# Kernel optimization log

Measured on AMD Instinct MI355X. Metric: run time of the kernel, lower is better.

The kernel has to match this reference:

```python
import jax, jax.numpy as jnp
import numpy as np

H = 400   # hidden_size
V = 77    # vocab / window size
K = 10    # attention mixture components
OUT = 121
B, T, U = 64, 600, 50


def setup_inputs() -> dict:
    key = jax.random.key(0)
    ks = jax.random.split(key, 16)
    def p(k, shape, s=0.08):
        return jax.random.normal(k, shape, dtype=jnp.float32) * s
    # bias for kappa-increment chunk kept negative so kappa advances ~exp(-3)=0.05/step
    b_win = jnp.concatenate([jnp.zeros(2 * K, jnp.float32), jnp.full((K,), -3.0, jnp.float32)])
    return {
        "inputs": jax.random.normal(ks[0], (B, T, 3), dtype=jnp.float32),
        "text": jax.random.randint(ks[1], (B, U), 0, V),
        "text_mask": jnp.ones((B, U), jnp.float32),
        "h0": jnp.zeros((3, B, H), jnp.float32),
        "c0": jnp.zeros((3, B, H), jnp.float32),
        "prev_window_vec": jnp.zeros((B, 1, V), jnp.float32),
        "prev_kappa": jnp.zeros((B, K, 1), jnp.float32),
        "w_ih1": p(ks[2], (4 * H, 3 + V)), "w_hh1": p(ks[3], (4 * H, H)),
        "b_ih1": jnp.zeros((4 * H,), jnp.float32), "b_hh1": jnp.zeros((4 * H,), jnp.float32),
        "w_ih2": p(ks[4], (4 * H, 3 + V + H)), "w_hh2": p(ks[5], (4 * H, H)),
        "b_ih2": jnp.zeros((4 * H,), jnp.float32), "b_hh2": jnp.zeros((4 * H,), jnp.float32),
        "w_ih3": p(ks[6], (4 * H, 3 + V + H)), "w_hh3": p(ks[7], (4 * H, H)),
        "b_ih3": jnp.zeros((4 * H,), jnp.float32), "b_hh3": jnp.zeros((4 * H,), jnp.float32),
        "w_win": p(ks[8], (3 * K, H), 0.01), "b_win": b_win,
        "w_out": p(ks[9], (OUT, 3 * H)), "b_out": jnp.zeros((OUT,), jnp.float32),
    }


def lstm_cell(x, h, c, Wih, Whh, bih, bhh):
    # PyTorch gate order: i, f, g, o
    g = x @ Wih.T + bih + h @ Whh.T + bhh
    i, f, gg, o = jnp.split(g, 4, axis=-1)
    c = jax.nn.sigmoid(f) * c + jax.nn.sigmoid(i) * jnp.tanh(gg)
    h = jax.nn.sigmoid(o) * jnp.tanh(c)
    return h, c


def reference(inputs, text, text_mask, h0, c0, prev_window_vec, prev_kappa,
              w_ih1, w_hh1, b_ih1, b_hh1, w_ih2, w_hh2, b_ih2, b_hh2,
              w_ih3, w_hh3, b_ih3, b_hh3, w_win, b_win, w_out, b_out):
    enc = jax.nn.one_hot(text, V, dtype=jnp.float32)            # [B,U,V]
    u = jnp.arange(U, dtype=jnp.float32)                         # [U]

    def step1(carry, x_t):
        h, c, wv, kappa = carry                                  # h,c:[B,H] wv:[B,V] kappa:[B,K]
        xi = jnp.concatenate([x_t, wv], axis=-1)                 # [B,3+V]
        h, c = lstm_cell(xi, h, c, w_ih1, w_hh1, b_ih1, b_hh1)
        mix = jnp.exp(h @ w_win.T + b_win)                       # [B,3K]
        alpha, beta, dk = jnp.split(mix, 3, axis=-1)             # each [B,K]
        kappa = kappa + dk
        phi = jnp.sum(alpha[:, :, None] * jnp.exp(-beta[:, :, None] * (kappa[:, :, None] - u) ** 2), axis=1)  # [B,U]
        phi = phi * text_mask
        wv = jnp.einsum('bu,buv->bv', phi, enc)                  # [B,V]
        return (h, c, wv, kappa), (h, wv)

    carry0 = (h0[0], c0[0], prev_window_vec[:, 0, :], prev_kappa[:, :, 0])
    (h1, c1, _, kappa_last), (hid1, wvec) = jax.lax.scan(step1, carry0, jnp.swapaxes(inputs, 0, 1))
    hid1 = jnp.swapaxes(hid1, 0, 1)                              # [B,T,H]
    wvec = jnp.swapaxes(wvec, 0, 1)                              # [B,T,V]

    def run_lstm(x, h, c, Wih, Whh, bih, bhh):
        def step(carry, x_t):
            h, c = carry
            h, c = lstm_cell(x_t, h, c, Wih, Whh, bih, bhh)
            return (h, c), h
        _, hs = jax.lax.scan(step, (h, c), jnp.swapaxes(x, 0, 1))
        return jnp.swapaxes(hs, 0, 1)

    hid2 = run_lstm(jnp.concatenate([inputs, hid1, wvec], axis=-1), h0[1], c0[1], w_ih2, w_hh2, b_ih2, b_hh2)
    hid3 = run_lstm(jnp.concatenate([inputs, hid2, wvec], axis=-1), h0[2], c0[2], w_ih3, w_hh3, b_ih3, b_hh3)
    y_hat = jnp.concatenate([hid1, hid2, hid3], axis=-1) @ w_out.T + b_out  # [B,T,121]
    return y_hat, wvec, kappa_last[:, :, None]
```

## Files before the change

kernel.cpp:

```cpp
#include <hip/hip_runtime.h>
#include <cstdint>
#include <cstddef>
#include <cstring>

using u32 = unsigned int;
typedef _Float16 h2 __attribute__((ext_vector_type(2)));
typedef _Float16 h4 __attribute__((ext_vector_type(4)));
typedef _Float16 h8 __attribute__((ext_vector_type(8)));
typedef float f32x4 __attribute__((ext_vector_type(4)));

constexpr int B_=64, T_=600, U_=50, V_=77, H_=400, OUT_=121;
constexpr int G1=50, GPA=16, G2=50, G3=50, GOUT=8;
constexpr int NBLK = G1+GPA+G2+G3+GOUT;
constexpr u32 CNT0=50, CNT1=16, CNT2=50, CNT3=50;

constexpr size_t FLAGS_B = 0;
constexpr size_t FLAGS_SZ = 4ull*600*64;
constexpr size_t W1WG   = 15ull*32*4*8;
constexpr size_t W1F_B  = FLAGS_SZ;
constexpr size_t W2WG   = 28ull*32*4*8;
constexpr size_t W2F_B  = W1F_B + 50ull*W1WG*2;
constexpr size_t W3F_B  = W2F_B + 50ull*W2WG*2;
constexpr size_t WOWG   = 300ull*32*16;
constexpr size_t WOF_B  = W3F_B + 50ull*W2WG*2;
constexpr size_t WWFWG  = 200ull*32;
constexpr size_t WWF_B  = WOF_B + 8ull*WOWG*2;
constexpr size_t WWMWG  = 15ull*32*4*8;
constexpr size_t WWM_B  = WWF_B + 16ull*WWFWG*4;
constexpr size_t FWV_B  = WWM_B + 50ull*WWMWG*2;
constexpr size_t FH1_B  = FWV_B + 600ull*64*40*4;
constexpr size_t FH2_B  = FH1_B + 600ull*64*200*4;
constexpr size_t FH3_B  = FH2_B + 600ull*64*200*4;

constexpr int SW1 = 184;
constexpr int SW2 = 232;
constexpr int SWO = 244;
constexpr int SMEM_BYTES = 59392;

struct P {
  const float *x, *tmask, *h0, *c0, *pwv, *pkap;
  const int *text;
  const float *wih1,*whh1,*bih1,*bhh1;
  const float *wih2,*whh2,*bih2,*bhh2;
  const float *wih3,*whh3,*bih3,*bhh3;
  const float *wwin,*bwin,*wout,*bout;
  float *out_y,*out_wv,*out_kap;
  _Float16 *w1f,*w2f,*w3f,*wof,*wwm;
  u32 *wwf;
  u32 *fwv,*fh1,*fh2,*fh3;
  u32 *flags;
};

__device__ __forceinline__ u32 ldc_u(const u32* p) {
  return __hip_atomic_load((u32*)p, __ATOMIC_RELAXED, __HIP_MEMORY_SCOPE_AGENT);
}
__device__ __forceinline__ void stc_u(u32* p, u32 v) {
  __hip_atomic_store(p, v, __ATOMIC_RELAXED, __HIP_MEMORY_SCOPE_AGENT);
}
__device__ __forceinline__ float sigm(float x) { return 1.f/(1.f+__expf(-x)); }
__device__ __forceinline__ h2 pk16(float a, float b) {
  auto t = __builtin_amdgcn_cvt_pkrtz(a, b);
  h2 r; memcpy(&r, &t, 4); return r;
}
__device__ __forceinline__ u32 h2u(h2 v) { u32 r; memcpy(&r, &v, 4); return r; }
__device__ __forceinline__ h2 u2h(u32 v) { h2 r; memcpy(&r, &v, 4); return r; }
__device__ __forceinline__ u32 pkf(float a, float b) { return h2u(pk16(a, b)); }
__device__ __forceinline__ float dot2(h2 a, h2 b, float c) { return __builtin_amdgcn_fdot2(a, b, c, false); }
__device__ __forceinline__ h2 lo4(h4 v) { return __builtin_shufflevector(v, v, 0, 1); }
__device__ __forceinline__ h2 hi4(h4 v) { return __builtin_shufflevector(v, v, 2, 3); }

__device__ __forceinline__ void wait_cnt(u32* cnt, int stage, int t, u32 target) {
  if (threadIdx.x == 0) {
    const u32* s = cnt + ((size_t)stage*600 + t)*16;
    while (ldc_u(s) < target) {}
  }
  __syncthreads();
}
__device__ __forceinline__ void add_cnt(u32* cnt, int stage, int t) {
  if (threadIdx.x == 0)
    (void)__hip_atomic_fetch_add(cnt + ((size_t)stage*600 + t)*16, 1u,
                                 __ATOMIC_RELAXED, __HIP_MEMORY_SCOPE_AGENT);
}

__device__ __forceinline__ void mfma_chunk5(const _Float16* pan, int SWf, const _Float16* WA,
                                            int w, int l, f32x4& acc0, f32x4& acc1) {
  const _Float16* bp0 = pan + ((w>>1)*32 + (l&15))*SWf + (l>>4)*8;
  const _Float16* bp1 = bp0 + 16*SWf;
  const _Float16* ap  = WA + (((16*(w&1) + (l&15))*4) + (l>>4))*8;
#pragma unroll
  for (int ks = 0; ks < 5; ++ks) {
    h8 a  = *(const h8*)(ap  + ks*1024);
    h8 b0 = *(const h8*)(bp0 + ks*32);
    h8 b1 = *(const h8*)(bp1 + ks*32);
    acc0 = __builtin_amdgcn_mfma_f32_16x16x32_f16(a, b0, acc0, 0, 0, 0);
    acc1 = __builtin_amdgcn_mfma_f32_16x16x32_f16(a, b1, acc1, 0, 0, 0);
  }
}
__device__ __forceinline__ void mfma_chunk7(const _Float16* pan, int SWf, const _Float16* WA,
                                            int w, int l, f32x4& acc0, f32x4& acc1) {
  const _Float16* bp0 = pan + ((w>>1)*32 + (l&15))*SWf + (l>>4)*8;
  const _Float16* bp1 = bp0 + 16*SWf;
  const _Float16* ap  = WA + (((16*(w&1) + (l&15))*4) + (l>>4))*8;
#pragma unroll
  for (int ks = 0; ks < 7; ++ks) {
    h8 a  = *(const h8*)(ap  + ks*1024);
    h8 b0 = *(const h8*)(bp0 + ks*32);
    h8 b1 = *(const h8*)(bp1 + ks*32);
    acc0 = __builtin_amdgcn_mfma_f32_16x16x32_f16(a, b0, acc0, 0, 0, 0);
    acc1 = __builtin_amdgcn_mfma_f32_16x16x32_f16(a, b1, acc1, 0, 0, 0);
  }
}

__device__ void lstm1_role(const P& p, int wg, char* smem) {
  const int tid = threadIdx.x;
  const int w = tid >> 6, l = tid & 63;
  const int ul = (w&1)*4 + (l>>4);
  const int u  = wg*8 + ul;
  const int bA = (w>>1)*32 + (l&15), bB = bA + 16;
  _Float16* panA = (_Float16*)smem;
  _Float16* panB = panA + 64*SW1;
  float* kapS = (float*)(smem + 47104);
  float* mixE = (float*)(smem + 49664);
  float* wvs  = (float*)(smem + 23552);
  _Float16* wgW = p.w1f + (size_t)wg * W1WG;
  _Float16* wgM = p.wwm + (size_t)wg * WWMWG;
  for (int e = tid; e < 15360; e += 256) {
    int i = e & 7, q = (e>>3)&3, row = (e>>5)&31, ks = e>>10;
    int k = ks*32 + q*8 + i;
    int cu = row>>2, g = row&3;
    int r = g*400 + wg*8 + cu;
    float v;
    if (k < 400)      v = p.whh1[(size_t)r*400 + k];
    else if (k < 477) v = p.wih1[(size_t)r*80 + 3 + (k-400)];
    else              v = p.wih1[(size_t)r*80 + (k-477)];
    wgW[e] = (_Float16)v;
  }
  for (int e = tid; e < 15360; e += 256) {
    int i = e & 7, q = (e>>3)&3, row = (e>>5)&31, ks = e>>10;
    int k = ks*32 + q*8 + i;
    float v = 0.f;
    if (row < 30 && k < 400) v = p.wwin[(size_t)row*400 + k];
    wgM[e] = (_Float16)v;
  }
  for (int i = tid; i < 640; i += 256) kapS[i] = p.pkap[i];
  float bsum[4];
#pragma unroll
  for (int g = 0; g < 4; ++g) bsum[g] = p.bih1[g*400+u] + p.bhh1[g*400+u];
  float creg[2];
  creg[0] = p.c0[(size_t)bA*H_ + u];
  creg[1] = p.c0[(size_t)bB*H_ + u];
  __syncthreads();

  for (int t = 0; t < T_; ++t) {
    f32x4 acc0 = {0.f,0.f,0.f,0.f}, acc1 = {0.f,0.f,0.f,0.f};
    f32x4 am0  = {0.f,0.f,0.f,0.f}, am1  = {0.f,0.f,0.f,0.f};
    if (t > 0) wait_cnt(p.flags, 0, t-1, CNT0); else __syncthreads();
    const u32* h1p = p.fh1 + (size_t)(t-1)*64*200;
    {
      u32 tmp[20];
#pragma unroll
      for (int it = 0; it < 20; ++it) {
        int idx = tid + it*256; int b = idx/80, q = idx - b*80;
        if (t == 0) { float2 f = *(const float2*)(p.h0 + (size_t)b*H_ + 2*q); tmp[it] = pkf(f.x, f.y); }
        else tmp[it] = h1p[b*200 + q];
      }
#pragma unroll
      for (int it = 0; it < 20; ++it) {
        int idx = tid + it*256; int b = idx/80, q = idx - b*80;
        ((u32*)panA)[b*92 + q] = tmp[it];
      }
    }
    __syncthreads();
    {
      u32 tmp[20];
#pragma unroll
      for (int it = 0; it < 20; ++it) {
        int idx = tid + it*256; int b = idx/80, q = 80 + (idx - b*80);
        if (t == 0) { float2 f = *(const float2*)(p.h0 + (size_t)b*H_ + 2*q); tmp[it] = pkf(f.x, f.y); }
        else tmp[it] = h1p[b*200 + q];
      }
      mfma_chunk5(panA, SW1, wgW, w, l, acc0, acc1);
      if (t > 0) mfma_chunk5(panA, SW1, wgM, w, l, am0, am1);
#pragma unroll
      for (int it = 0; it < 20; ++it) {
        int idx = tid + it*256; int b = idx/80, q = idx - b*80;
        ((u32*)panB)[b*92 + q] = tmp[it];
      }
    }
    __syncthreads();
    {
      u32 tmp[10], tw[10];
#pragma unroll
      for (int it = 0; it < 10; ++it) {
        int idx = tid + it*256; int b = idx/40, q = idx - b*40;
        if (t == 0) { float2 f = *(const float2*)(p.h0 + (size_t)b*H_ + 2*(160+q)); tmp[it] = pkf(f.x, f.y); }
        else tmp[it] = h1p[b*200 + 160 + q];
        if (t == 0) {
          u32 v;
          if (q < 38)       v = pkf(p.pwv[(size_t)b*V_ + 2*q], p.pwv[(size_t)b*V_ + 2*q + 1]);
          else if (q == 38) v = pkf(p.pwv[(size_t)b*V_ + 76], p.x[((size_t)b*T_ + t)*3 + 0]);
          else              v = pkf(p.x[((size_t)b*T_ + t)*3 + 1], p.x[((size_t)b*T_ + t)*3 + 2]);
          tw[it] = v;
        } else tw[it] = 0u;
      }
      mfma_chunk5(panB, SW1, wgW + 5*1024, w, l, acc0, acc1);
      if (t > 0) mfma_chunk5(panB, SW1, wgM + 5*1024, w, l, am0, am1);
#pragma unroll
      for (int it = 0; it < 10; ++it) {
        int idx = tid + it*256; int b = idx/40, q = idx - b*40;
        ((u32*)panA)[b*92 + q] = tmp[it];
        ((u32*)panA)[b*92 + 40 + q] = tw[it];
      }
    }
    __syncthreads();
    if (t > 0) {
      for (int i = tid; i < 4928; i += 256) wvs[i] = 0.f;
      mfma_chunk5(panA, SW1, wgM + 10*1024, w, l, am0, am1);
#pragma unroll
      for (int r = 0; r < 4; ++r) {
        int m = 16*(w&1) + (l>>4)*4 + r;
        if (m < 30) {
          float e0 = __expf(am0[r] + p.bwin[m]);
          float e1 = __expf(am1[r] + p.bwin[m]);
          mixE[bA*32 + m] = e0;
          mixE[bB*32 + m] = e1;
          if (m >= 20) { kapS[bA*10 + (m-20)] += e0; kapS[bB*10 + (m-20)] += e1; }
        }
      }
      __syncthreads();
      for (int c = tid; c < 3200; c += 256) {
        int b = c/50, uu = c - (c/50)*50;
        const float fu = (float)uu;
        float s = 0.f;
#pragma unroll
        for (int k = 0; k < 10; ++k) {
          float df = kapS[b*10+k] - fu;
          s += mixE[b*32+k] * __expf(-mixE[b*32+10+k]*df*df);
        }
        s *= p.tmask[(size_t)b*U_ + uu];
        atomicAdd(&wvs[b*77 + p.text[(size_t)b*U_ + uu]], s);
      }
      __syncthreads();
      for (int i = tid; i < 2560; i += 256) {
        int b = i/40, q = i - (i/40)*40;
        u32 v;
        if (q < 38)       v = pkf(wvs[b*77 + 2*q], wvs[b*77 + 2*q + 1]);
        else if (q == 38) v = pkf(wvs[b*77 + 76], p.x[((size_t)b*T_ + t)*3 + 0]);
        else              v = pkf(p.x[((size_t)b*T_ + t)*3 + 1], p.x[((size_t)b*T_ + t)*3 + 2]);
        ((u32*)panA)[b*92 + 40 + q] = v;
      }
      __syncthreads();
    }
    mfma_chunk5(panA, SW1, wgW + 10*1024, w, l, acc0, acc1);

    float hA, hB;
    {
      float cn = sigm(acc0[1]+bsum[1])*creg[0] + sigm(acc0[0]+bsum[0])*tanhf(acc0[2]+bsum[2]);
      creg[0] = cn; hA = sigm(acc0[3]+bsum[3])*tanhf(cn);
      float cn2 = sigm(acc1[1]+bsum[1])*creg[1] + sigm(acc1[0]+bsum[0])*tanhf(acc1[2]+bsum[2]);
      creg[1] = cn2; hB = sigm(acc1[3]+bsum[3])*tanhf(cn2);
    }
    {
      float hAp = __shfl_xor(hA, 16, 64);
      float hBp = __shfl_xor(hB, 16, 64);
      if (((l>>4) & 1) == 0) {
        const int pi = wg*4 + (ul>>1);
        stc_u(p.fh1 + ((size_t)t*64 + bA)*200 + pi, pkf(hA, hAp));
        stc_u(p.fh1 + ((size_t)t*64 + bB)*200 + pi, pkf(hB, hBp));
      }
    }
    __syncthreads();
    add_cnt(p.flags, 0, t);
  }
}

__device__ void pa_role(const P& p, int pa, char* smem) {
  const int tid = threadIdx.x;
  const int b0p = pa*4;
  u32* hsm    = (u32*)smem;
  float* mixP = (float*)(smem + 3200);
  float* mixL = (float*)(smem + 4160);
  float* kapL = (float*)(smem + 4640);
  float* wvs  = (float*)(smem + 4800);
  int* textL  = (int*)(smem + 6032);
  u32* wwf = p.wwf + (size_t)pa * WWFWG;
  for (int e = tid; e < 200*30; e += 256) {
    int kk = e / 30, m = e - (e/30)*30;
    wwf[(size_t)kk*32 + m] = pkf(p.wwin[(size_t)m*400 + 2*kk], p.wwin[(size_t)m*400 + 2*kk + 1]);
  }
  for (int i = tid; i < 200; i += 256)
    textL[i] = p.text[(size_t)(b0p + i/50)*U_ + (i - (i/50)*50)];
  float kap_reg = 0.f;
  if (tid < 120 && (tid % 30) >= 20)
    kap_reg = p.pkap[(size_t)(b0p + tid/30)*10 + (tid % 30 - 20)];
  __syncthreads();

  for (int t = 0; t < T_; ++t) {
    wait_cnt(p.flags, 0, t, CNT0);
    for (int e = tid; e < 800; e += 256) {
      int bl = e / 200, q = e - bl*200;
      hsm[e] = p.fh1[((size_t)t*64 + b0p + bl)*200 + q];
    }
    for (int i = tid; i < 308; i += 256) wvs[i] = 0.f;
    __syncthreads();
    if (tid < 240) {
      int pp = tid >> 1, h = tid & 1;
      int bl = pp / 30, m = pp - bl*30;
      const u32* hp = hsm + bl*200 + h*100;
      const u32* wp = wwf + (size_t)(h*100)*32 + m;
      float d0=0.f, d1=0.f, d2=0.f, d3=0.f;
#pragma unroll 4
      for (int kk = 0; kk < 100; kk += 4) {
        d0 = dot2(u2h(hp[kk]),   u2h(wp[(size_t)kk*32]),     d0);
        d1 = dot2(u2h(hp[kk+1]), u2h(wp[(size_t)(kk+1)*32]), d1);
        d2 = dot2(u2h(hp[kk+2]), u2h(wp[(size_t)(kk+2)*32]), d2);
        d3 = dot2(u2h(hp[kk+3]), u2h(wp[(size_t)(kk+3)*32]), d3);
      }
      mixP[tid] = (d0+d1)+(d2+d3);
    }
    __syncthreads();
    if (tid < 120) {
      int bl = tid / 30, m = tid - bl*30;
      float v = __expf(mixP[2*tid] + mixP[2*tid+1] + p.bwin[m]);
      mixL[tid] = v;
      if (m >= 20) {
        kap_reg += v;
        kapL[bl*10 + (m-20)] = kap_reg;
        if (t == T_-1) p.out_kap[(size_t)(b0p+bl)*10 + (m-20)] = kap_reg;
      }
    }
    __syncthreads();
    if (tid < 200) {
      int bl = tid / 50, uu = tid - bl*50;
      const float fu = (float)uu;
      float s = 0.f;
#pragma unroll
      for (int k = 0; k < 10; ++k) {
        float df = kapL[bl*10+k] - fu;
        s += mixL[bl*30+k] * __expf(-mixL[bl*30+10+k]*df*df);
      }
      s *= p.tmask[(size_t)(b0p+bl)*U_ + uu];
      atomicAdd(&wvs[bl*77 + textL[tid]], s);
    }
    __syncthreads();
    for (int i = tid; i < 308; i += 256) {
      int bl = i / 77, v = i - (i/77)*77;
      p.out_wv[((size_t)(b0p+bl)*T_ + t)*V_ + v] = wvs[i];
    }
    for (int i = tid; i < 160; i += 256) {
      int bl = i / 40, pr = i - (i/40)*40;
      int b = b0p + bl;
      float f0, f1;
      if (pr < 38)       { f0 = wvs[bl*77 + 2*pr]; f1 = wvs[bl*77 + 2*pr + 1]; }
      else if (pr == 38) { f0 = wvs[bl*77 + 76];   f1 = p.x[((size_t)b*T_ + t)*3 + 0]; }
      else               { f0 = p.x[((size_t)b*T_ + t)*3 + 1]; f1 = p.x[((size_t)b*T_ + t)*3 + 2]; }
      stc_u(p.fwv + ((size_t)t*64 + b)*40 + pr, pkf(f0, f1));
    }
    __syncthreads();
    add_cnt(p.flags, 1, t);
  }
}

__device__ __forceinline__ void stage_l23(u32* pan, int tid, int ph, int t,
    const u32* fwvt, const u32* hint, const u32* rect, const float* h0f) {
  u32 tmp[28];
#pragma unroll
  for (int it = 0; it < 28; ++it) {
    int idx = tid + it*256;
    int b = idx/112, pl = idx - b*112;
    int gp = ph*112 + pl;
    u32 v;
    if (gp < 40) v = fwvt[b*40 + gp];
    else if (gp < 240) v = hint[b*200 + gp - 40];
    else if (gp < 440) {
      if (t == 0) { float2 f = *(const float2*)(h0f + (size_t)b*H_ + 2*(gp-240)); v = pkf(f.x, f.y); }
      else v = rect[b*200 + gp - 240];
    } else v = 0u;
    tmp[it] = v;
  }
#pragma unroll
  for (int it = 0; it < 28; ++it) {
    int idx = tid + it*256;
    int b = idx/112, pl = idx - b*112;
    pan[b*116 + pl] = tmp[it];
  }
}

template <int L>
__device__ void lstm_role(const P& p, int wg, char* smem) {
  const int tid = threadIdx.x;
  const int w = tid >> 6, l = tid & 63;
  const int ul = (w&1)*4 + (l>>4);
  const int u  = wg*8 + ul;
  const int bA = (w>>1)*32 + (l&15), bB = bA + 16;
  constexpr int STG = (L==2) ? 2 : 3;
  _Float16* wgW = ((L==2) ? p.w2f : p.w3f) + (size_t)wg * W2WG;
  const float* wih = (L==2) ? p.wih2 : p.wih3;
  const float* whh = (L==2) ? p.whh2 : p.whh3;
  const float* bih = (L==2) ? p.bih2 : p.bih3;
  const float* bhh = (L==2) ? p.bhh2 : p.bhh3;
  const u32* hin = (L==2) ? p.fh1 : p.fh2;
  u32* rec = (L==2) ? p.fh2 : p.fh3;
  _Float16* panA = (_Float16*)smem;
  _Float16* panB = panA + 64*SW2;

  for (int e = tid; e < 28672; e += 256) {
    int i = e & 7, q = (e>>3)&3, row = (e>>5)&31, ks = e>>10;
    int k = ks*32 + q*8 + i;
    int cu = row>>2, g = row&3;
    int r = g*400 + wg*8 + cu;
    float v;
    if (k < 77)       v = wih[(size_t)r*480 + 403 + k];
    else if (k < 80)  v = wih[(size_t)r*480 + (k-77)];
    else if (k < 480) v = wih[(size_t)r*480 + 3 + (k-80)];
    else if (k < 880) v = whh[(size_t)r*400 + (k-480)];
    else              v = 0.f;
    wgW[e] = (_Float16)v;
  }
  float bsum[4];
#pragma unroll
  for (int g = 0; g < 4; ++g) bsum[g] = bih[g*400+u] + bhh[g*400+u];
  float creg[2];
  creg[0] = p.c0[(size_t)(L-1)*B_*H_ + (size_t)bA*H_ + u];
  creg[1] = p.c0[(size_t)(L-1)*B_*H_ + (size_t)bB*H_ + u];
  __syncthreads();

  for (int t = 0; t < T_; ++t) {
    f32x4 acc0 = {0.f,0.f,0.f,0.f}, acc1 = {0.f,0.f,0.f,0.f};
    if (L == 2) wait_cnt(p.flags, 1, t, CNT1);
    else        wait_cnt(p.flags, 2, t, CNT2);
    const u32* fwvt = p.fwv + (size_t)t*64*40;
    const u32* hint = hin + (size_t)t*64*200;
    const u32* rect = rec + (size_t)(t-1)*64*200;
    const float* h0f = p.h0 + (size_t)(L-1)*B_*H_;
    stage_l23((u32*)panA, tid, 0, t, fwvt, hint, rect, h0f);
    __syncthreads();
    {
      u32 tmp[28];
#pragma unroll
      for (int it = 0; it < 28; ++it) {
        int idx = tid + it*256;
        int b = idx/112, pl = idx - b*112;
        tmp[it] = hint[b*200 + 72 + pl];
      }
      mfma_chunk7(panA, SW2, wgW, w, l, acc0, acc1);
#pragma unroll
      for (int it = 0; it < 28; ++it) {
        int idx = tid + it*256;
        int b = idx/112, pl = idx - b*112;
        ((u32*)panB)[b*116 + pl] = tmp[it];
      }
    }
    if (t > 0) wait_cnt(p.flags, STG, t-1, CNT2); else __syncthreads();
    {
      u32 tmp[28];
#pragma unroll
      for (int it = 0; it < 28; ++it) {
        int idx = tid + it*256;
        int b = idx/112, pl = idx - b*112;
        int gp = 224 + pl;
        u32 v;
        if (gp < 240) v = hint[b*200 + gp - 40];
        else if (t == 0) { float2 f = *(const float2*)(h0f + (size_t)b*H_ + 2*(gp-240)); v = pkf(f.x, f.y); }
        else v = rect[b*200 + gp - 240];
        tmp[it] = v;
      }
      mfma_chunk7(panB, SW2, wgW + 7*1024, w, l, acc0, acc1);
#pragma unroll
      for (int it = 0; it < 28; ++it) {
        int idx = tid + it*256;
        int b = idx/112, pl = idx - b*112;
        ((u32*)panA)[b*116 + pl] = tmp[it];
      }
    }
    __syncthreads();
    {
      u32 tmp[28];
#pragma unroll
      for (int it = 0; it < 28; ++it) {
        int idx = tid + it*256;
        int b = idx/112, pl = idx - b*112;
        int gp = 336 + pl;
        u32 v;
        if (gp < 440) {
          if (t == 0) { float2 f = *(const float2*)(h0f + (size_t)b*H_ + 2*(gp-240)); v = pkf(f.x, f.y); }
          else v = rect[b*200 + gp - 240];
        } else v = 0u;
        tmp[it] = v;
      }
      mfma_chunk7(panA, SW2, wgW + 14*1024, w, l, acc0, acc1);
#pragma unroll
      for (int it = 0; it < 28; ++it) {
        int idx = tid + it*256;
        int b = idx/112, pl = idx - b*112;
        ((u32*)panB)[b*116 + pl] = tmp[it];
      }
    }
    __syncthreads();
    mfma_chunk7(panB, SW2, wgW + 21*1024, w, l, acc0, acc1);

    float hA, hB;
    {
      float cn = sigm(acc0[1]+bsum[1])*creg[0] + sigm(acc0[0]+bsum[0])*tanhf(acc0[2]+bsum[2]);
      creg[0] = cn; hA = sigm(acc0[3]+bsum[3])*tanhf(cn);
      float cn2 = sigm(acc1[1]+bsum[1])*creg[1] + sigm(acc1[0]+bsum[0])*tanhf(acc1[2]+bsum[2]);
      creg[1] = cn2; hB = sigm(acc1[3]+bsum[3])*tanhf(cn2);
    }
    {
      float hAp = __shfl_xor(hA, 16, 64);
      float hBp = __shfl_xor(hB, 16, 64);
      if (((l>>4) & 1) == 0) {
        const int pi = wg*4 + (ul>>1);
        stc_u(rec + ((size_t)t*64 + bA)*200 + pi, pkf(hA, hAp));
        stc_u(rec + ((size_t)t*64 + bB)*200 + pi, pkf(hB, hBp));
      }
    }
    __syncthreads();
    add_cnt(p.flags, STG, t);
  }
}

__device__ void out_role(const P& p, int g, char* smem) {
  const int tid = threadIdx.x;
  const int cg = tid & 31, bg = tid >> 5;
  const int c0 = cg*4;
  _Float16* pan = (_Float16*)smem;
  _Float16* wofg = p.wof + (size_t)g*WOWG;
  for (int e = tid; e < 300*32*16; e += 256) {
    int kk = e >> 9, rem = e & 511;
    int cgi = rem >> 4, j4 = rem & 15;
    int j = j4 >> 2, kc = j4 & 3;
    int c = cgi*4 + j; if (c > 120) c = 120;
    wofg[e] = (_Float16)p.wout[(size_t)c*1200 + kk*4 + kc];
  }
  float bo[4];
#pragma unroll
  for (int j = 0; j < 4; ++j) {
    int c = c0 + j; if (c > 120) c = 120;
    bo[j] = p.bout[c];
  }
  __syncthreads();

  for (int t = g; t < T_; t += GOUT) {
    wait_cnt(p.flags, 3, t, CNT3);
    float acc[8][4];
#pragma unroll
    for (int r = 0; r < 8; ++r)
#pragma unroll
      for (int j = 0; j < 4; ++j) acc[r][j] = 0.f;

    for (int ph = 0; ph < 5; ++ph) {
      for (int idx = tid; idx < 7680; idx += 256) {
        int b = idx / 120, pl = idx - b*120;
        int Pp = ph*120 + pl;
        u32 pv;
        if (Pp < 200)      pv = p.fh1[((size_t)t*64 + b)*200 + Pp];
        else if (Pp < 400) pv = p.fh2[((size_t)t*64 + b)*200 + (Pp-200)];
        else               pv = p.fh3[((size_t)t*64 + b)*200 + (Pp-400)];
        ((u32*)pan)[b*122 + pl] = pv;
      }
      __syncthreads();
      const _Float16* wp = wofg + ((size_t)(ph*60)*32 + cg)*16;
#pragma unroll 3
      for (int k = 0; k < 240; k += 4) {
        h4 wa = *(const h4*)(wp);
        h4 wb = *(const h4*)(wp+4);
        h4 wc = *(const h4*)(wp+8);
        h4 wd = *(const h4*)(wp+12);
        wp += 512;
#pragma unroll
        for (int r = 0; r < 8; ++r) {
          h4 a = *(const h4*)(pan + (bg*8+r)*SWO + k);
          h2 al = lo4(a), ah = hi4(a);
          acc[r][0] = dot2(al, lo4(wa), acc[r][0]); acc[r][0] = dot2(ah, hi4(wa), acc[r][0]);
          acc[r][1] = dot2(al, lo4(wb), acc[r][1]); acc[r][1] = dot2(ah, hi4(wb), acc[r][1]);
          acc[r][2] = dot2(al, lo4(wc), acc[r][2]); acc[r][2] = dot2(ah, hi4(wc), acc[r][2]);
          acc[r][3] = dot2(al, lo4(wd), acc[r][3]); acc[r][3] = dot2(ah, hi4(wd), acc[r][3]);
        }
      }
      __syncthreads();
    }
#pragma unroll
    for (int r = 0; r < 8; ++r)
#pragma unroll
      for (int j = 0; j < 4; ++j) {
        int c = c0 + j;
        if (c < 121)
          p.out_y[((size_t)(bg*8+r)*T_ + t)*OUT_ + c] = acc[r][j] + bo[j];
      }
    __syncthreads();
  }
}

__global__ __launch_bounds__(256) void hw_pipeline(P p) {
  __shared__ __align__(16) char smem_raw[SMEM_BYTES];
  const int bid = blockIdx.x;
  if (bid < G1) lstm1_role(p, bid, smem_raw);
  else if (bid < G1+GPA) pa_role(p, bid - G1, smem_raw);
  else if (bid < G1+GPA+G2) lstm_role<2>(p, bid - G1 - GPA, smem_raw);
  else if (bid < G1+GPA+G2+G3) lstm_role<3>(p, bid - G1 - GPA - G2, smem_raw);
  else out_role(p, bid - G1 - GPA - G2 - G3, smem_raw);
}

extern "C" void kernel_launch(void* const* d_in, const int* in_sizes, int n_in,
                              void* d_out, int out_size, void* d_ws, size_t ws_size,
                              hipStream_t stream) {
  (void)in_sizes; (void)n_in; (void)out_size; (void)ws_size;
  P p;
  p.x = (const float*)d_in[0];
  p.text = (const int*)d_in[1];
  p.tmask = (const float*)d_in[2];
  p.h0 = (const float*)d_in[3];
  p.c0 = (const float*)d_in[4];
  p.pwv = (const float*)d_in[5];
  p.pkap = (const float*)d_in[6];
  p.wih1 = (const float*)d_in[7];  p.whh1 = (const float*)d_in[8];
  p.bih1 = (const float*)d_in[9];  p.bhh1 = (const float*)d_in[10];
  p.wih2 = (const float*)d_in[11]; p.whh2 = (const float*)d_in[12];
  p.bih2 = (const float*)d_in[13]; p.bhh2 = (const float*)d_in[14];
  p.wih3 = (const float*)d_in[15]; p.whh3 = (const float*)d_in[16];
  p.bih3 = (const float*)d_in[17]; p.bhh3 = (const float*)d_in[18];
  p.wwin = (const float*)d_in[19]; p.bwin = (const float*)d_in[20];
  p.wout = (const float*)d_in[21]; p.bout = (const float*)d_in[22];
  float* out = (float*)d_out;
  p.out_y  = out;
  p.out_wv = out + (size_t)B_*T_*OUT_;
  p.out_kap = p.out_wv + (size_t)B_*T_*V_;
  char* ws = (char*)d_ws;
  p.flags = (u32*)(ws + FLAGS_B);
  p.w1f = (_Float16*)(ws + W1F_B);
  p.w2f = (_Float16*)(ws + W2F_B);
  p.w3f = (_Float16*)(ws + W3F_B);
  p.wof = (_Float16*)(ws + WOF_B);
  p.wwm = (_Float16*)(ws + WWM_B);
  p.wwf = (u32*)(ws + WWF_B);
  p.fwv = (u32*)(ws + FWV_B);
  p.fh1 = (u32*)(ws + FH1_B);
  p.fh2 = (u32*)(ws + FH2_B);
  p.fh3 = (u32*)(ws + FH3_B);
  (void)hipMemsetAsync(ws + FLAGS_B, 0, FLAGS_SZ, stream);
  hipLaunchKernelGGL(hw_pipeline, dim3(NBLK), dim3(256), 0, stream, p);
}
```

Before: 15.51 ms.

## Consolidate LSTM layers onto fewer workgroups with per-producer flag barriers

Each LSTM layer's work now runs on 10 workgroups instead of 50. Every workgroup handles 5 row tiles (40 hidden units), and the h panel staged in shared memory is reused across all 5 tiles. The atomic-counter barrier is replaced by per-producer flags that consumers poll in parallel with s_sleep. The window-mixture weights are shared by all workgroups instead of copied per workgroup. The aim is to cut cross-workgroup sync traffic and redundant panel loads on the serial timestep chain, at the cost of 5x more MFMA work per workgroup per step, more register pressure, and a longer critical path within each workgroup.

```diff
diff --git a/kernel.cpp b/kernel.cpp
--- a/kernel.cpp
+++ b/kernel.cpp
@@ -10,24 +10,23 @@
 typedef float f32x4 __attribute__((ext_vector_type(4)));
 
 constexpr int B_=64, T_=600, U_=50, V_=77, H_=400, OUT_=121;
-constexpr int G1=50, GPA=16, G2=50, G3=50, GOUT=8;
+constexpr int G1=10, GPA=16, G2=10, G3=10, GOUT=8;
 constexpr int NBLK = G1+GPA+G2+G3+GOUT;
-constexpr u32 CNT0=50, CNT1=16, CNT2=50, CNT3=50;
+constexpr int RT_ = 5;
 
 constexpr size_t FLAGS_B = 0;
-constexpr size_t FLAGS_SZ = 4ull*600*64;
-constexpr size_t W1WG   = 15ull*32*4*8;
+constexpr size_t FLAGS_SZ = 4ull*600*16*32;
+constexpr size_t W1WG   = (size_t)RT_*15*32*4*8;
 constexpr size_t W1F_B  = FLAGS_SZ;
-constexpr size_t W2WG   = 28ull*32*4*8;
-constexpr size_t W2F_B  = W1F_B + 50ull*W1WG*2;
-constexpr size_t W3F_B  = W2F_B + 50ull*W2WG*2;
+constexpr size_t W2WG   = (size_t)RT_*28*32*4*8;
+constexpr size_t W2F_B  = W1F_B + 10ull*W1WG*2;
+constexpr size_t W3F_B  = W2F_B + 10ull*W2WG*2;
 constexpr size_t WOWG   = 300ull*32*16;
-constexpr size_t WOF_B  = W3F_B + 50ull*W2WG*2;
+constexpr size_t WOF_B  = W3F_B + 10ull*W2WG*2;
 constexpr size_t WWFWG  = 200ull*32;
 constexpr size_t WWF_B  = WOF_B + 8ull*WOWG*2;
-constexpr size_t WWMWG  = 15ull*32*4*8;
 constexpr size_t WWM_B  = WWF_B + 16ull*WWFWG*4;
-constexpr size_t FWV_B  = WWM_B + 50ull*WWMWG*2;
+constexpr size_t FWV_B  = WWM_B + 15360ull*2;
 constexpr size_t FH1_B  = FWV_B + 600ull*64*40*4;
 constexpr size_t FH2_B  = FH1_B + 600ull*64*200*4;
 constexpr size_t FH3_B  = FH2_B + 600ull*64*200*4;
@@ -69,17 +68,16 @@
 __device__ __forceinline__ h2 lo4(h4 v) { return __builtin_shufflevector(v, v, 0, 1); }
 __device__ __forceinline__ h2 hi4(h4 v) { return __builtin_shufflevector(v, v, 2, 3); }
 
-__device__ __forceinline__ void wait_cnt(u32* cnt, int stage, int t, u32 target) {
-  if (threadIdx.x == 0) {
-    const u32* s = cnt + ((size_t)stage*600 + t)*16;
-    while (ldc_u(s) < target) {}
+__device__ __forceinline__ void wait_flags(u32* f, int stage, int t, int n) {
+  if ((int)threadIdx.x < n) {
+    const u32* s = f + (((size_t)stage*600 + t)*16 + threadIdx.x)*8;
+    while (ldc_u(s) == 0) __builtin_amdgcn_s_sleep(1);
   }
   __syncthreads();
 }
-__device__ __forceinline__ void add_cnt(u32* cnt, int stage, int t) {
+__device__ __forceinline__ void set_flag(u32* f, int stage, int t, int prod) {
   if (threadIdx.x == 0)
-    (void)__hip_atomic_fetch_add(cnt + ((size_t)stage*600 + t)*16, 1u,
-                                 __ATOMIC_RELAXED, __HIP_MEMORY_SCOPE_AGENT);
+    stc_u(f + (((size_t)stage*600 + t)*16 + prod)*8, 1u);
 }
 
 __device__ __forceinline__ void mfma_chunk5(const _Float16* pan, int SWf, const _Float16* WA,
@@ -114,8 +112,7 @@
 __device__ void lstm1_role(const P& p, int wg, char* smem) {
   const int tid = threadIdx.x;
   const int w = tid >> 6, l = tid & 63;
-  const int ul = (w&1)*4 + (l>>4);
-  const int u  = wg*8 + ul;
+  const int ulb = (w&1)*4 + (l>>4);
   const int bA = (w>>1)*32 + (l&15), bB = bA + 16;
   _Float16* panA = (_Float16*)smem;
   _Float16* panB = panA + 64*SW1;
@@ -123,12 +120,13 @@
   float* mixE = (float*)(smem + 49664);
   float* wvs  = (float*)(smem + 23552);
   _Float16* wgW = p.w1f + (size_t)wg * W1WG;
-  _Float16* wgM = p.wwm + (size_t)wg * WWMWG;
-  for (int e = tid; e < 15360; e += 256) {
-    int i = e & 7, q = (e>>3)&3, row = (e>>5)&31, ks = e>>10;
+  _Float16* wgM = p.wwm;
+  for (int e = tid; e < RT_*15360; e += 256) {
+    int rt = e / 15360, e2 = e - rt*15360;
+    int i = e2 & 7, q = (e2>>3)&3, row = (e2>>5)&31, ks = e2>>10;
     int k = ks*32 + q*8 + i;
     int cu = row>>2, g = row&3;
-    int r = g*400 + wg*8 + cu;
+    int r = g*400 + wg*40 + rt*8 + cu;
     float v;
     if (k < 400)      v = p.whh1[(size_t)r*400 + k];
     else if (k < 477) v = p.wih1[(size_t)r*80 + 3 + (k-400)];
@@ -143,18 +141,24 @@
     wgM[e] = (_Float16)v;
   }
   for (int i = tid; i < 640; i += 256) kapS[i] = p.pkap[i];
-  float bsum[4];
-#pragma unroll
-  for (int g = 0; g < 4; ++g) bsum[g] = p.bih1[g*400+u] + p.bhh1[g*400+u];
-  float creg[2];
-  creg[0] = p.c0[(size_t)bA*H_ + u];
-  creg[1] = p.c0[(size_t)bB*H_ + u];
+  float bsum[RT_][4];
+  float creg[RT_][2];
+#pragma unroll
+  for (int rt = 0; rt < RT_; ++rt) {
+    int u = wg*40 + rt*8 + ulb;
+#pragma unroll
+    for (int g = 0; g < 4; ++g) bsum[rt][g] = p.bih1[g*400+u] + p.bhh1[g*400+u];
+    creg[rt][0] = p.c0[(size_t)bA*H_ + u];
+    creg[rt][1] = p.c0[(size_t)bB*H_ + u];
+  }
   __syncthreads();
 
   for (int t = 0; t < T_; ++t) {
-    f32x4 acc0 = {0.f,0.f,0.f,0.f}, acc1 = {0.f,0.f,0.f,0.f};
-    f32x4 am0  = {0.f,0.f,0.f,0.f}, am1  = {0.f,0.f,0.f,0.f};
-    if (t > 0) wait_cnt(p.flags, 0, t-1, CNT0); else __syncthreads();
+    f32x4 accA[RT_], accB[RT_];
+#pragma unroll
+    for (int rt = 0; rt < RT_; ++rt) { accA[rt] = {0.f,0.f,0.f,0.f}; accB[rt] = {0.f,0.f,0.f,0.f}; }
+    f32x4 am0 = {0.f,0.f,0.f,0.f}, am1 = {0.f,0.f,0.f,0.f};
+    if (t > 0) wait_flags(p.flags, 0, t-1, G1); else __syncthreads();
     const u32* h1p = p.fh1 + (size_t)(t-1)*64*200;
     {
       u32 tmp[20];
@@ -179,7 +183,9 @@
         if (t == 0) { float2 f = *(const float2*)(p.h0 + (size_t)b*H_ + 2*q); tmp[it] = pkf(f.x, f.y); }
         else tmp[it] = h1p[b*200 + q];
       }
-      mfma_chunk5(panA, SW1, wgW, w, l, acc0, acc1);
+#pragma unroll
+      for (int rt = 0; rt < RT_; ++rt)
+        mfma_chunk5(panA, SW1, wgW + (size_t)rt*15360, w, l, accA[rt], accB[rt]);
       if (t > 0) mfma_chunk5(panA, SW1, wgM, w, l, am0, am1);
 #pragma unroll
       for (int it = 0; it < 20; ++it) {
@@ -203,8 +209,10 @@
           tw[it] = v;
         } else tw[it] = 0u;
       }
-      mfma_chunk5(panB, SW1, wgW + 5*1024, w, l, acc0, acc1);
-      if (t > 0) mfma_chunk5(panB, SW1, wgM + 5*1024, w, l, am0, am1);
+#pragma unroll
+      for (int rt = 0; rt < RT_; ++rt)
+        mfma_chunk5(panB, SW1, wgW + (size_t)rt*15360 + 5120, w, l, accA[rt], accB[rt]);
+      if (t > 0) mfma_chunk5(panB, SW1, wgM + 5120, w, l, am0, am1);
 #pragma unroll
       for (int it = 0; it < 10; ++it) {
         int idx = tid + it*256; int b = idx/40, q = idx - b*40;
@@ -215,7 +223,7 @@
     __syncthreads();
     if (t > 0) {
       for (int i = tid; i < 4928; i += 256) wvs[i] = 0.f;
-      mfma_chunk5(panA, SW1, wgM + 10*1024, w, l, am0, am1);
+      mfma_chunk5(panA, SW1, wgM + 10240, w, l, am0, am1);
 #pragma unroll
       for (int r = 0; r < 4; ++r) {
         int m = 16*(w&1) + (l>>4)*4 + r;
@@ -251,26 +259,29 @@
       }
       __syncthreads();
     }
-    mfma_chunk5(panA, SW1, wgW + 10*1024, w, l, acc0, acc1);
-
-    float hA, hB;
-    {
-      float cn = sigm(acc0[1]+bsum[1])*creg[0] + sigm(acc0[0]+bsum[0])*tanhf(acc0[2]+bsum[2]);
-      creg[0] = cn; hA = sigm(acc0[3]+bsum[3])*tanhf(cn);
-      float cn2 = sigm(acc1[1]+bsum[1])*creg[1] + sigm(acc1[0]+bsum[0])*tanhf(acc1[2]+bsum[2]);
-      creg[1] = cn2; hB = sigm(acc1[3]+bsum[3])*tanhf(cn2);
-    }
-    {
+#pragma unroll
+    for (int rt = 0; rt < RT_; ++rt)
+      mfma_chunk5(panA, SW1, wgW + (size_t)rt*15360 + 10240, w, l, accA[rt], accB[rt]);
+
+#pragma unroll
+    for (int rt = 0; rt < RT_; ++rt) {
+      float hA, hB;
+      {
+        float cn = sigm(accA[rt][1]+bsum[rt][1])*creg[rt][0] + sigm(accA[rt][0]+bsum[rt][0])*tanhf(accA[rt][2]+bsum[rt][2]);
+        creg[rt][0] = cn; hA = sigm(accA[rt][3]+bsum[rt][3])*tanhf(cn);
+        float cn2 = sigm(accB[rt][1]+bsum[rt][1])*creg[rt][1] + sigm(accB[rt][0]+bsum[rt][0])*tanhf(accB[rt][2]+bsum[rt][2]);
+        creg[rt][1] = cn2; hB = sigm(accB[rt][3]+bsum[rt][3])*tanhf(cn2);
+      }
       float hAp = __shfl_xor(hA, 16, 64);
       float hBp = __shfl_xor(hB, 16, 64);
       if (((l>>4) & 1) == 0) {
-        const int pi = wg*4 + (ul>>1);
+        const int pi = wg*20 + rt*4 + (ulb>>1);
         stc_u(p.fh1 + ((size_t)t*64 + bA)*200 + pi, pkf(hA, hAp));
         stc_u(p.fh1 + ((size_t)t*64 + bB)*200 + pi, pkf(hB, hBp));
       }
     }
     __syncthreads();
-    add_cnt(p.flags, 0, t);
+    set_flag(p.flags, 0, t, wg);
   }
 }
 
@@ -296,7 +307,7 @@
   __syncthreads();
 
   for (int t = 0; t < T_; ++t) {
-    wait_cnt(p.flags, 0, t, CNT0);
+    wait_flags(p.flags, 0, t, G1);
     for (int e = tid; e < 800; e += 256) {
       int bl = e / 200, q = e - bl*200;
       hsm[e] = p.fh1[((size_t)t*64 + b0p + bl)*200 + q];
@@ -357,7 +368,7 @@
       stc_u(p.fwv + ((size_t)t*64 + b)*40 + pr, pkf(f0, f1));
     }
     __syncthreads();
-    add_cnt(p.flags, 1, t);
+    set_flag(p.flags, 1, t, pa);
   }
 }
 
@@ -390,8 +401,7 @@
 __device__ void lstm_role(const P& p, int wg, char* smem) {
   const int tid = threadIdx.x;
   const int w = tid >> 6, l = tid & 63;
-  const int ul = (w&1)*4 + (l>>4);
-  const int u  = wg*8 + ul;
+  const int ulb = (w&1)*4 + (l>>4);
   const int bA = (w>>1)*32 + (l&15), bB = bA + 16;
   constexpr int STG = (L==2) ? 2 : 3;
   _Float16* wgW = ((L==2) ? p.w2f : p.w3f) + (size_t)wg * W2WG;
@@ -404,11 +414,12 @@
   _Float16* panA = (_Float16*)smem;
   _Float16* panB = panA + 64*SW2;
 
-  for (int e = tid; e < 28672; e += 256) {
-    int i = e & 7, q = (e>>3)&3, row = (e>>5)&31, ks = e>>10;
+  for (int e = tid; e < RT_*28672; e += 256) {
+    int rt = e / 28672, e2 = e - rt*28672;
+    int i = e2 & 7, q = (e2>>3)&3, row = (e2>>5)&31, ks = e2>>10;
     int k = ks*32 + q*8 + i;
     int cu = row>>2, g = row&3;
-    int r = g*400 + wg*8 + cu;
+    int r = g*400 + wg*40 + rt*8 + cu;
     float v;
     if (k < 77)       v = wih[(size_t)r*480 + 403 + k];
     else if (k < 80)  v = wih[(size_t)r*480 + (k-77)];
@@ -417,18 +428,24 @@
     else              v = 0.f;
     wgW[e] = (_Float16)v;
   }
-  float bsum[4];
-#pragma unroll
-  for (int g = 0; g < 4; ++g) bsum[g] = bih[g*400+u] + bhh[g*400+u];
-  float creg[2];
-  creg[0] = p.c0[(size_t)(L-1)*B_*H_ + (size_t)bA*H_ + u];
-  creg[1] = p.c0[(size_t)(L-1)*B_*H_ + (size_t)bB*H_ + u];
+  float bsum[RT_][4];
+  float creg[RT_][2];
+#pragma unroll
+  for (int rt = 0; rt < RT_; ++rt) {
+    int u = wg*40 + rt*8 + ulb;
+#pragma unroll
+    for (int g = 0; g < 4; ++g) bsum[rt][g] = bih[g*400+u] + bhh[g*400+u];
+    creg[rt][0] = p.c0[(size_t)(L-1)*B_*H_ + (size_t)bA*H_ + u];
+    creg[rt][1] = p.c0[(size_t)(L-1)*B_*H_ + (size_t)bB*H_ + u];
+  }
   __syncthreads();
 
   for (int t = 0; t < T_; ++t) {
-    f32x4 acc0 = {0.f,0.f,0.f,0.f}, acc1 = {0.f,0.f,0.f,0.f};
-    if (L == 2) wait_cnt(p.flags, 1, t, CNT1);
-    else        wait_cnt(p.flags, 2, t, CNT2);
+    f32x4 accA[RT_], accB[RT_];
+#pragma unroll
+    for (int rt = 0; rt < RT_; ++rt) { accA[rt] = {0.f,0.f,0.f,0.f}; accB[rt] = {0.f,0.f,0.f,0.f}; }
+    if (L == 2) wait_flags(p.flags, 1, t, GPA);
+    else        wait_flags(p.flags, 2, t, G2);
     const u32* fwvt = p.fwv + (size_t)t*64*40;
     const u32* hint = hin + (size_t)t*64*200;
     const u32* rect = rec + (size_t)(t-1)*64*200;
@@ -443,7 +460,9 @@
         int b = idx/112, pl = idx - b*112;
         tmp[it] = hint[b*200 + 72 + pl];
       }
-      mfma_chunk7(panA, SW2, wgW, w, l, acc0, acc1);
+#pragma unroll
+      for (int rt = 0; rt < RT_; ++rt)
+        mfma_chunk7(panA, SW2, wgW + (size_t)rt*28672, w, l, accA[rt], accB[rt]);
 #pragma unroll
       for (int it = 0; it < 28; ++it) {
         int idx = tid + it*256;
@@ -451,7 +470,7 @@
         ((u32*)panB)[b*116 + pl] = tmp[it];
       }
     }
-    if (t > 0) wait_cnt(p.flags, STG, t-1, CNT2); else __syncthreads();
+    if (t > 0) wait_flags(p.flags, STG, t-1, (L==2)?G2:G3); else __syncthreads();
     {
       u32 tmp[28];
 #pragma unroll
@@ -465,7 +484,9 @@
         else v = rect[b*200 + gp - 240];
         tmp[it] = v;
       }
-      mfma_chunk7(panB, SW2, wgW + 7*1024, w, l, acc0, acc1);
+#pragma unroll
+      for (int rt = 0; rt < RT_; ++rt)
+        mfma_chunk7(panB, SW2, wgW + (size_t)rt*28672 + 7168, w, l, accA[rt], accB[rt]);
 #pragma unroll
       for (int it = 0; it < 28; ++it) {
         int idx = tid + it*256;
@@ -488,7 +509,9 @@
         } else v = 0u;
         tmp[it] = v;
       }
-      mfma_chunk7(panA, SW2, wgW + 14*1024, w, l, acc0, acc1);
+#pragma unroll
+      for (int rt = 0; rt < RT_; ++rt)
+        mfma_chunk7(panA, SW2, wgW + (size_t)rt*28672 + 14336, w, l, accA[rt], accB[rt]);
 #pragma unroll
       for (int it = 0; it < 28; ++it) {
         int idx = tid + it*256;
@@ -497,26 +520,29 @@
       }
     }
     __syncthreads();
-    mfma_chunk7(panB, SW2, wgW + 21*1024, w, l, acc0, acc1);
-
-    float hA, hB;
-    {
-      float cn = sigm(acc0[1]+bsum[1])*creg[0] + sigm(acc0[0]+bsum[0])*tanhf(acc0[2]+bsum[2]);
-      creg[0] = cn; hA = sigm(acc0[3]+bsum[3])*tanhf(cn);
-      float cn2 = sigm(acc1[1]+bsum[1])*creg[1] + sigm(acc1[0]+bsum[0])*tanhf(acc1[2]+bsum[2]);
-      creg[1] = cn2; hB = sigm(acc1[3]+bsum[3])*tanhf(cn2);
-    }
-    {
+#pragma unroll
+    for (int rt = 0; rt < RT_; ++rt)
+      mfma_chunk7(panB, SW2, wgW + (size_t)rt*28672 + 21504, w, l, accA[rt], accB[rt]);
+
+#pragma unroll
+    for (int rt = 0; rt < RT_; ++rt) {
+      float hA, hB;
+      {
+        float cn = sigm(accA[rt][1]+bsum[rt][1])*creg[rt][0] + sigm(accA[rt][0]+bsum[rt][0])*tanhf(accA[rt][2]+bsum[rt][2]);
+        creg[rt][0] = cn; hA = sigm(accA[rt][3]+bsum[rt][3])*tanhf(cn);
+        float cn2 = sigm(accB[rt][1]+bsum[rt][1])*creg[rt][1] + sigm(accB[rt][0]+bsum[rt][0])*tanhf(accB[rt][2]+bsum[rt][2]);
+        creg[rt][1] = cn2; hB = sigm(accB[rt][3]+bsum[rt][3])*tanhf(cn2);
+      }
       float hAp = __shfl_xor(hA, 16, 64);
       float hBp = __shfl_xor(hB, 16, 64);
       if (((l>>4) & 1) == 0) {
-        const int pi = wg*4 + (ul>>1);
+        const int pi = wg*20 + rt*4 + (ulb>>1);
         stc_u(rec + ((size_t)t*64 + bA)*200 + pi, pkf(hA, hAp));
         stc_u(rec + ((size_t)t*64 + bB)*200 + pi, pkf(hB, hBp));
       }
     }
     __syncthreads();
-    add_cnt(p.flags, STG, t);
+    set_flag(p.flags, STG, t, wg);
   }
 }
 
@@ -542,7 +568,7 @@
   __syncthreads();
 
   for (int t = g; t < T_; t += GOUT) {
-    wait_cnt(p.flags, 3, t, CNT3);
+    wait_flags(p.flags, 3, t, G3);
     float acc[8][4];
 #pragma unroll
     for (int r = 0; r < 8; ++r)
@@ -592,7 +618,7 @@
   }
 }
 
-__global__ __launch_bounds__(256) void hw_pipeline(P p) {
+__global__ __launch_bounds__(256, 1) void hw_pipeline(P p) {
   __shared__ __align__(16) char smem_raw[SMEM_BYTES];
   const int bid = blockIdx.x;
   if (bid < G1) lstm1_role(p, bid, smem_raw);
```

Result: slower. 31.24 ms (+101.4%).

## Replace atomic counters with per-producer flags polled in parallel

Applied to the files above, without the earlier changes.

Inter-block synchronization changes from a single atomic counter per (stage, timestep), incremented by every producer workgroup, to a separate flag slot per producer. Each slot sits on its own 16-byte stride, and consumers poll all producer flags in parallel with one thread per producer, adding s_sleep backoff between polls. The aim is to remove contention from serialized atomic increments on one cache line and shorten the critical path of the recurrent pipeline. In exchange the flag buffer grows sixteenfold, and polling traffic from many threads could add memory pressure.

```diff
diff --git a/kernel.cpp b/kernel.cpp
--- a/kernel.cpp
+++ b/kernel.cpp
@@ -12,10 +12,9 @@
 constexpr int B_=64, T_=600, U_=50, V_=77, H_=400, OUT_=121;
 constexpr int G1=50, GPA=16, G2=50, G3=50, GOUT=8;
 constexpr int NBLK = G1+GPA+G2+G3+GOUT;
-constexpr u32 CNT0=50, CNT1=16, CNT2=50, CNT3=50;
 
 constexpr size_t FLAGS_B = 0;
-constexpr size_t FLAGS_SZ = 4ull*600*64;
+constexpr size_t FLAGS_SZ = 4ull*600*64*16;
 constexpr size_t W1WG   = 15ull*32*4*8;
 constexpr size_t W1F_B  = FLAGS_SZ;
 constexpr size_t W2WG   = 28ull*32*4*8;
@@ -69,17 +68,16 @@
 __device__ __forceinline__ h2 lo4(h4 v) { return __builtin_shufflevector(v, v, 0, 1); }
 __device__ __forceinline__ h2 hi4(h4 v) { return __builtin_shufflevector(v, v, 2, 3); }
 
-__device__ __forceinline__ void wait_cnt(u32* cnt, int stage, int t, u32 target) {
-  if (threadIdx.x == 0) {
-    const u32* s = cnt + ((size_t)stage*600 + t)*16;
-    while (ldc_u(s) < target) {}
+__device__ __forceinline__ void wait_flags(u32* f, int stage, int t, int n) {
+  if ((int)threadIdx.x < n) {
+    const u32* s = f + (((size_t)stage*600 + t)*64 + threadIdx.x)*4;
+    while (ldc_u(s) == 0) __builtin_amdgcn_s_sleep(2);
   }
   __syncthreads();
 }
-__device__ __forceinline__ void add_cnt(u32* cnt, int stage, int t) {
+__device__ __forceinline__ void set_flag(u32* f, int stage, int t, int prod) {
   if (threadIdx.x == 0)
-    (void)__hip_atomic_fetch_add(cnt + ((size_t)stage*600 + t)*16, 1u,
-                                 __ATOMIC_RELAXED, __HIP_MEMORY_SCOPE_AGENT);
+    stc_u(f + (((size_t)stage*600 + t)*64 + prod)*4, 1u);
 }
 
 __device__ __forceinline__ void mfma_chunk5(const _Float16* pan, int SWf, const _Float16* WA,
@@ -154,7 +152,7 @@
   for (int t = 0; t < T_; ++t) {
     f32x4 acc0 = {0.f,0.f,0.f,0.f}, acc1 = {0.f,0.f,0.f,0.f};
     f32x4 am0  = {0.f,0.f,0.f,0.f}, am1  = {0.f,0.f,0.f,0.f};
-    if (t > 0) wait_cnt(p.flags, 0, t-1, CNT0); else __syncthreads();
+    if (t > 0) wait_flags(p.flags, 0, t-1, G1); else __syncthreads();
     const u32* h1p = p.fh1 + (size_t)(t-1)*64*200;
     {
       u32 tmp[20];
@@ -270,7 +268,7 @@
       }
     }
     __syncthreads();
-    add_cnt(p.flags, 0, t);
+    set_flag(p.flags, 0, t, wg);
   }
 }
 
@@ -296,7 +294,7 @@
   __syncthreads();
 
   for (int t = 0; t < T_; ++t) {
-    wait_cnt(p.flags, 0, t, CNT0);
+    wait_flags(p.flags, 0, t, G1);
     for (int e = tid; e < 800; e += 256) {
       int bl = e / 200, q = e - bl*200;
       hsm[e] = p.fh1[((size_t)t*64 + b0p + bl)*200 + q];
@@ -357,7 +355,7 @@
       stc_u(p.fwv + ((size_t)t*64 + b)*40 + pr, pkf(f0, f1));
     }
     __syncthreads();
-    add_cnt(p.flags, 1, t);
+    set_flag(p.flags, 1, t, pa);
   }
 }
 
@@ -427,8 +425,8 @@
 
   for (int t = 0; t < T_; ++t) {
     f32x4 acc0 = {0.f,0.f,0.f,0.f}, acc1 = {0.f,0.f,0.f,0.f};
-    if (L == 2) wait_cnt(p.flags, 1, t, CNT1);
-    else        wait_cnt(p.flags, 2, t, CNT2);
+    if (L == 2) wait_flags(p.flags, 1, t, GPA);
+    else        wait_flags(p.flags, 2, t, G2);
     const u32* fwvt = p.fwv + (size_t)t*64*40;
     const u32* hint = hin + (size_t)t*64*200;
     const u32* rect = rec + (size_t)(t-1)*64*200;
@@ -451,7 +449,7 @@
         ((u32*)panB)[b*116 + pl] = tmp[it];
       }
     }
-    if (t > 0) wait_cnt(p.flags, STG, t-1, CNT2); else __syncthreads();
+    if (t > 0) wait_flags(p.flags, STG, t-1, (L==2)?G2:G3); else __syncthreads();
     {
       u32 tmp[28];
 #pragma unroll
@@ -516,7 +514,7 @@
       }
     }
     __syncthreads();
-    add_cnt(p.flags, STG, t);
+    set_flag(p.flags, STG, t, wg);
   }
 }
 
@@ -542,7 +540,7 @@
   __syncthreads();
 
   for (int t = g; t < T_; t += GOUT) {
-    wait_cnt(p.flags, 3, t, CNT3);
+    wait_flags(p.flags, 3, t, G3);
     float acc[8][4];
 #pragma unroll
     for (int r = 0; r < 8; ++r)
```

Measured after the change: 14.51 ms. -6.4%, faster.
